# Optimization experiments

Hardware: AMD Instinct MI355X
Metric: run time of the kernel (lower is better)

Reference implementation:

```python
import jax, jax.numpy as jnp
import numpy as np

NUM_TOKENS = 4096
LATENT_DIM = 256
BETA = 0.25
TEMPERATURE = 1.0  # temp_init buffer value
EPS_TEMP = 1e-6


def setup_inputs() -> dict:
    key = jax.random.key(0)
    k1, k2 = jax.random.split(key)
    latent = jax.random.normal(k1, (4, 2048, LATENT_DIM), dtype=jnp.float32)
    cb = jax.random.normal(k2, (NUM_TOKENS, LATENT_DIM), dtype=jnp.float32)
    # module normalizes codebook rows at init
    codebook = cb / jnp.linalg.norm(cb, axis=-1, keepdims=True)
    return {"latent": latent, "codebook": codebook}


def _l2norm(x):
    return x / jnp.clip(jnp.linalg.norm(x, axis=-1, keepdims=True), 1e-12)


def reference(latent, codebook):
    B, S, D = latent.shape
    flat = latent.reshape(-1, D)                       # [N, D]
    # cosine similarity via normalized matmul
    ln = _l2norm(flat)
    cn = _l2norm(codebook)
    cosine_sim = jnp.einsum('nd,kd->nk', ln, cn)       # [N, K]
    distances = 2.0 - 2.0 * cosine_sim
    scaled = distances / jnp.maximum(TEMPERATURE, EPS_TEMP)
    soft_assign = jax.nn.softmax(-scaled, axis=-1)     # [N, K]
    indices = jnp.argmax(soft_assign, axis=-1)         # [N]
    hard_assign = jax.nn.one_hot(indices, NUM_TOKENS, dtype=jnp.float32)
    # straight-through soft->hard assignment
    assign = hard_assign + soft_assign - jax.lax.stop_gradient(soft_assign)

    selected_cosine_sim = jnp.take_along_axis(cosine_sim, indices[:, None], axis=1).mean()

    # codebook pairwise euclidean diagnostics (off-diagonal mean / min)
    sq = jnp.sum(codebook * codebook, axis=-1)         # [K]
    d2 = sq[:, None] + sq[None, :] - 2.0 * (codebook @ codebook.T)
    cdist = jnp.sqrt(jnp.clip(d2, 0.0))                # [K, K]
    K = NUM_TOKENS
    off_sum = jnp.sum(cdist) - jnp.sum(jnp.diagonal(cdist))
    avg_euclidean = off_sum / (K * (K - 1))
    eye = jnp.eye(K, dtype=bool)
    min_euclidean = jnp.min(jnp.where(eye, jnp.inf, cdist))

    quantized = (assign @ codebook).reshape(B, S, D)
    commitment_loss = BETA * jnp.mean((jax.lax.stop_gradient(latent) - quantized) ** 2)
    codebook_loss = jnp.mean((latent - jax.lax.stop_gradient(quantized)) ** 2)
    quantized = latent + jax.lax.stop_gradient(quantized - latent)

    avg_probs = jnp.mean(hard_assign, axis=0)
    perplexity = jnp.exp(-jnp.sum(avg_probs * jnp.log(avg_probs + 1e-10)))

    return (quantized, indices, commitment_loss, codebook_loss, perplexity,
            selected_cosine_sim, avg_euclidean, min_euclidean)
```

## Files before the change

kernel.cpp:

```cpp
#include <hip/hip_runtime.h>
#include <hip/hip_bf16.h>
#include <math.h>

#define NTOK 8192
#define DIM 256
#define KCB 4096
#define NCB (KCB / 128)
#define NKEY 4
#define NKROW (NCB * NKEY)
#define DELTA 0.08f
#define GTIE 2e-6
#define MAXC 16
#define NPAIRB (NCB * (NCB + 1) / 2)
#define NSCOB (NCB * (NTOK / 128))

typedef unsigned long long ull;
typedef unsigned short ushort;
typedef __attribute__((ext_vector_type(8))) short shortx8;
typedef __attribute__((ext_vector_type(4))) float floatx4;
typedef const __attribute__((address_space(1))) void* gas_cp;
typedef __attribute__((address_space(3))) void* las_p;

__device__ __forceinline__ unsigned f2ord(float f) {
    unsigned u = __float_as_uint(f);
    return (u & 0x80000000u) ? ~u : (u | 0x80000000u);
}
__device__ __forceinline__ float ord2f(unsigned u) {
    unsigned b = (u & 0x80000000u) ? (u & 0x7FFFFFFFu) : ~u;
    return __uint_as_float(b);
}
__device__ __forceinline__ ushort f2bf(float f) {
    unsigned u = __float_as_uint(f);
    unsigned r = u + 0x7FFFu + ((u >> 16) & 1u);
    return (ushort)(r >> 16);
}

union TileSmem {
    struct { ushort a[128][64]; ushort b[128][64]; } t;
    unsigned keys[128][33];
    struct { float rs[128]; float rm[128]; } red;
};

__device__ __forceinline__ void stage_tile(const ushort* __restrict__ gbase,
                                           ushort (*lds)[64], int wave, int lane,
                                           int kk) {
    int p = lane & 7;
    int rsub = lane >> 3;
    int kc = p ^ (rsub & 7);
    const ushort* src0 = gbase + (size_t)(wave * 64 + rsub) * DIM + kk + kc * 8;
#pragma unroll
    for (int c = 0; c < 8; ++c) {
        const ushort* src = src0 + (size_t)(c * 8) * DIM;
        __builtin_amdgcn_global_load_lds((gas_cp)src, (las_p)&lds[wave * 64 + c * 8][0],
                                         16, 0, 0);
    }
}
__device__ __forceinline__ shortx8 frag_read(const ushort (*lds)[64], int row,
                                             int lc) {
    return *(const shortx8*)&lds[row][(lc ^ (row & 7)) * 8];
}

__device__ __forceinline__ float np_combine(const float* racc) {
    float h0 = __fadd_rn(__fadd_rn(__fadd_rn(racc[0], racc[1]), __fadd_rn(racc[2], racc[3])),
                         __fadd_rn(__fadd_rn(racc[4], racc[5]), __fadd_rn(racc[6], racc[7])));
    float h1 = __fadd_rn(__fadd_rn(__fadd_rn(racc[8], racc[9]), __fadd_rn(racc[10], racc[11])),
                         __fadd_rn(__fadd_rn(racc[12], racc[13]), __fadd_rn(racc[14], racc[15])));
    float s = __fadd_rn(h0, h1);
    return fmaxf(sqrtf(s), 1e-12f);
}

__global__ __launch_bounds__(256) void prep(const float* __restrict__ lat,
                                            const float* __restrict__ cb,
                                            float* __restrict__ nrml,
                                            float* __restrict__ nrmc,
                                            ushort* __restrict__ latbf,
                                            ushort* __restrict__ cnbf,
                                            ushort* __restrict__ cbbf,
                                            float* __restrict__ sq,
                                            unsigned* __restrict__ counts) {
    int bid = blockIdx.x, t = threadIdx.x;
    if (bid < NTOK) {
        int n = bid;
        if (n < KCB / 256) counts[n * 256 + t] = 0u;
        const float* row = lat + (size_t)n * DIM;
        latbf[(size_t)n * DIM + t] = f2bf(row[t]);
        __shared__ float racc[16];
        if (t < 16) {
            int h = t >> 3, j = t & 7;
            const float* p = row + h * 128;
            float r = __fmul_rn(p[j], p[j]);
#pragma unroll 1
            for (int i = 8; i < 128; i += 8)
                r = __fadd_rn(r, __fmul_rn(p[i + j], p[i + j]));
            racc[t] = r;
        }
        __syncthreads();
        if (t == 0) nrml[n] = np_combine(racc);
    } else {
        int n = bid - NTOK;
        __shared__ float racc2[16];
        __shared__ double dacc[16];
        __shared__ float snrm;
        const float* row = cb + (size_t)n * DIM;
        if (t < 16) {
            int h = t >> 3, j = t & 7;
            const float* p = row + h * 128;
            float r = __fmul_rn(p[j], p[j]);
            double ds = 0.0;
#pragma unroll 1
            for (int i = 8; i < 128; i += 8)
                r = __fadd_rn(r, __fmul_rn(p[i + j], p[i + j]));
#pragma unroll 1
            for (int i = 0; i < 128; i += 8) { double v = (double)p[i + j]; ds += v * v; }
            racc2[t] = r; dacc[t] = ds;
        }
        __syncthreads();
        if (t == 0) {
            float nr = np_combine(racc2);
            snrm = nr; nrmc[n] = nr;
            double ds = 0.0;
            for (int i = 0; i < 16; ++i) ds += dacc[i];
            sq[n] = (float)ds;
        }
        __syncthreads();
        float c = row[t];
        cnbf[(size_t)n * DIM + t] = f2bf(c / snrm);
        cbbf[(size_t)n * DIM + t] = f2bf(c);
    }
}

__global__ __launch_bounds__(128, 2) void gemms(const ushort* __restrict__ latbf,
                                                const ushort* __restrict__ cnbf,
                                                const ushort* __restrict__ cbbf,
                                                const float* __restrict__ sq,
                                                unsigned* __restrict__ keysw,
                                                float* __restrict__ psumw,
                                                unsigned* __restrict__ pminw) {
    __shared__ TileSmem sm;
    int tid = threadIdx.x;
    int wave = tid >> 6, lane = tid & 63;
    int quad = lane >> 4, l15 = lane & 15;
    int wrow = wave * 64;
    bool isScore = blockIdx.x < NSCOB;
    int rowBase, colBase, tri = 0;
    const ushort *gA, *gB;
    if (isScore) {
        int cbk = blockIdx.x & (NCB - 1);
        int rbk = blockIdx.x >> 5;
        rowBase = rbk * 128; colBase = cbk * 128;
        gA = latbf + (size_t)rowBase * DIM;
        gB = cnbf + (size_t)colBase * DIM;
    } else {
        tri = blockIdx.x - NSCOB;
        int a = (int)((sqrtf(8.f * tri + 1.f) - 1.f) * 0.5f);
        while ((a + 1) * (a + 2) / 2 <= tri) ++a;
        while (a * (a + 1) / 2 > tri) --a;
        int b = tri - a * (a + 1) / 2;
        rowBase = b * 128; colBase = a * 128;
        gA = cbbf + (size_t)rowBase * DIM;
        gB = cbbf + (size_t)colBase * DIM;
    }
    floatx4 acc[4][8];
#pragma unroll
    for (int m = 0; m < 4; ++m)
#pragma unroll
        for (int n = 0; n < 8; ++n) acc[m][n] = (floatx4){0.f, 0.f, 0.f, 0.f};
#pragma unroll 1
    for (int kk = 0; kk < DIM; kk += 64) {
        __syncthreads();
        stage_tile(gA, sm.t.a, wave, lane, kk);
        stage_tile(gB, sm.t.b, wave, lane, kk);
        __syncthreads();
#pragma unroll
        for (int s = 0; s < 2; ++s) {
            shortx8 af[4];
#pragma unroll
            for (int mt = 0; mt < 4; ++mt)
                af[mt] = frag_read(sm.t.a, wrow + mt * 16 + l15, s * 4 + quad);
#pragma unroll
            for (int nt = 0; nt < 8; ++nt) {
                shortx8 bfr = frag_read(sm.t.b, nt * 16 + l15, s * 4 + quad);
#pragma unroll
                for (int mt = 0; mt < 4; ++mt)
                    acc[mt][nt] = __builtin_amdgcn_mfma_f32_16x16x32_bf16(
                        af[mt], bfr, acc[mt][nt], 0, 0, 0);
            }
        }
    }
    __syncthreads();
    if (isScore) {
        unsigned colp[8];
#pragma unroll
        for (int nt = 0; nt < 8; ++nt)
            colp[nt] = 4095u - (unsigned)(colBase + nt * 16 + l15);
#pragma unroll
        for (int mt = 0; mt < 4; ++mt)
#pragma unroll
            for (int reg = 0; reg < 4; ++reg) {
                unsigned b1 = 0u, b2 = 0u;
#pragma unroll
                for (int nt = 0; nt < 8; ++nt) {
                    unsigned key = (f2ord(acc[mt][nt][reg]) & 0xFFFFF000u) | colp[nt];
                    unsigned lo = min(key, b1);
                    b1 = max(key, b1);
                    b2 = max(lo, b2);
                }
                int row = wrow + mt * 16 + quad * 4 + reg;
                uint2 kv; kv.x = b1; kv.y = b2;
                *(uint2*)&sm.keys[row][l15 * 2] = kv;
            }
        __syncthreads();
        {
            unsigned a0 = 0, a1 = 0, a2 = 0, a3 = 0;
#pragma unroll
            for (int j = 0; j < 8; ++j) {
                uint4 v4 = *(const uint4*)&sm.keys[tid][j * 4];
                unsigned vs[4] = {v4.x, v4.y, v4.z, v4.w};
#pragma unroll
                for (int q = 0; q < 4; ++q) {
                    unsigned v = vs[q];
                    unsigned n0 = min(v, a0); a0 = max(v, a0);
                    unsigned n1 = min(n0, a1); a1 = max(n0, a1);
                    unsigned n2 = min(n1, a2); a2 = max(n1, a2);
                    a3 = max(n2, a3);
                }
            }
            size_t base = (size_t)(rowBase + tid) * NKROW + (blockIdx.x & (NCB - 1)) * NKEY;
            uint4 o; o.x = a0; o.y = a1; o.z = a2; o.w = a3;
            *(uint4*)&keysw[base] = o;
        }
    } else {
        float lsum = 0.f, lmin = INFINITY;
#pragma unroll
        for (int mt = 0; mt < 4; ++mt)
#pragma unroll
            for (int reg = 0; reg < 4; ++reg) {
                int i = rowBase + wrow + mt * 16 + quad * 4 + reg;
                float sqi = sq[i];
#pragma unroll
                for (int nt = 0; nt < 8; ++nt) {
                    int j = colBase + nt * 16 + l15;
                    float d2 = sqi + sq[j] - 2.0f * acc[mt][nt][reg];
                    float d = sqrtf(fmaxf(d2, 0.0f));
                    bool use = i < j;
                    lsum += use ? d : 0.f;
                    lmin = fminf(lmin, use ? d : INFINITY);
                }
            }
        sm.red.rs[tid] = lsum; sm.red.rm[tid] = lmin; __syncthreads();
        for (int s = 64; s > 0; s >>= 1) {
            if (tid < s) {
                sm.red.rs[tid] += sm.red.rs[tid + s];
                sm.red.rm[tid] = fminf(sm.red.rm[tid], sm.red.rm[tid + s]);
            }
            __syncthreads();
        }
        if (tid == 0) { psumw[tri] = sm.red.rs[0]; pminw[tri] = f2ord(sm.red.rm[0]); }
    }
}

__global__ __launch_bounds__(256) void argmax_resolve(const float* __restrict__ lat,
                                                      const float* __restrict__ cb,
                                                      const float* __restrict__ nrml,
                                                      const float* __restrict__ nrmc,
                                                      const unsigned* __restrict__ keysw,
                                                      float* __restrict__ outidx,
                                                      float* __restrict__ outq,
                                                      unsigned* __restrict__ counts,
                                                      float* __restrict__ selw,
                                                      float* __restrict__ msew) {
    __shared__ int scand[4][MAXC];
    __shared__ double sc64[4][MAXC];
    int wid = threadIdx.x >> 6, lane = threadIdx.x & 63;
    int n = blockIdx.x * 4 + wid;
    const unsigned* kr = keysw + (size_t)n * NKROW;
    uint2 kv = *(const uint2*)(kr + lane * 2);
    unsigned m = max(kv.x, kv.y);
#pragma unroll
    for (int off = 1; off < 64; off <<= 1) {
        unsigned o = __shfl_xor(m, off, 64);
        m = max(m, o);
    }
    float v1 = ord2f(m & 0xFFFFF000u);
    float thresh = v1 - DELTA;
    bool p0 = ord2f(kv.x & 0xFFFFF000u) >= thresh;
    bool p1 = ord2f(kv.y & 0xFFFFF000u) >= thresh;
    ull b0 = __ballot(p0), b1 = __ballot(p1);
    int below0 = __builtin_amdgcn_mbcnt_hi((unsigned)(b0 >> 32),
                 __builtin_amdgcn_mbcnt_lo((unsigned)b0, 0));
    int below1 = __builtin_amdgcn_mbcnt_hi((unsigned)(b1 >> 32),
                 __builtin_amdgcn_mbcnt_lo((unsigned)b1, 0));
    int base1 = __popcll(b0);
    int nc = base1 + __popcll(b1);
    if (p0 && below0 < MAXC)
        scand[wid][below0] = 4095 - (int)(kv.x & 0xFFFu);
    if (p1 && base1 + below1 < MAXC)
        scand[wid][base1 + below1] = 4095 - (int)(kv.y & 0xFFFu);
    nc = nc < MAXC ? nc : MAXC;
    __threadfence_block();
    float nx = nrml[n];
    int d0 = lane * 4;
    float4 xv = *(const float4*)(lat + (size_t)n * DIM + d0);
    int idx; float selcos;
    if (nc <= 1) {
        idx = 4095 - (int)(m & 0xFFFu);
        selcos = v1 / nx;
    } else {
        float la0 = xv.x / nx, la1 = xv.y / nx, la2 = xv.z / nx, la3 = xv.w / nx;
        for (int c = 0; c < nc; ++c) {
            int k = scand[wid][c];
            float nk = nrmc[k];
            float4 cv = *(const float4*)(cb + (size_t)k * DIM + d0);
            double part = (double)(cv.x / nk) * la0 + (double)(cv.y / nk) * la1 +
                          (double)(cv.z / nk) * la2 + (double)(cv.w / nk) * la3;
#pragma unroll
            for (int off = 1; off < 64; off <<= 1) part += __shfl_xor(part, off, 64);
            if (lane == 0) sc64[wid][c] = part;
        }
        __threadfence_block();
        double best64 = -1e300;
        for (int c = 0; c < nc; ++c) best64 = fmax(best64, sc64[wid][c]);
        int nrisk = 0;
        for (int c = 0; c < nc; ++c) if (sc64[wid][c] >= best64 - GTIE) ++nrisk;
        if (nrisk == 1) {
            idx = 0x7FFFFFFF; selcos = 0.f;
            for (int c = 0; c < nc; ++c)
                if (sc64[wid][c] >= best64 - GTIE) { idx = scand[wid][c]; selcos = (float)sc64[wid][c]; }
        } else {
            ull keyf = 0ull, keym = 0ull;
            if (lane < nc && sc64[wid][lane] >= best64 - GTIE) {
                int k = scand[wid][lane];
                const float* cr = cb + (size_t)k * DIM;
                const float* x = lat + (size_t)n * DIM;
                float nk = nrmc[k];
                float af = 0.f, am = 0.f;
                for (int d = 0; d < DIM; ++d) {
                    float la = x[d] / nx;
                    float cv = cr[d] / nk;
                    af = fmaf(la, cv, af);
                    am = __fadd_rn(am, __fmul_rn(la, cv));
                }
                float df = __fsub_rn(2.0f, __fmul_rn(2.0f, af));
                float dm = __fsub_rn(2.0f, __fmul_rn(2.0f, am));
                keyf = ((ull)(0xFFFFFFFFu - f2ord(df)) << 32) | (ull)(0xFFFFFFFFu - (unsigned)k);
                keym = ((ull)(0xFFFFFFFFu - f2ord(dm)) << 32) | (ull)(0xFFFFFFFFu - (unsigned)k);
            }
#pragma unroll
            for (int off = 1; off < 64; off <<= 1) {
                ull of = __shfl_xor(keyf, off, 64);
                ull om = __shfl_xor(keym, off, 64);
                keyf = of > keyf ? of : keyf;
                keym = om > keym ? om : keym;
            }
            int colf = (int)(0xFFFFFFFFu - (unsigned)(keyf & 0xFFFFFFFFull));
            int colm = (int)(0xFFFFFFFFu - (unsigned)(keym & 0xFFFFFFFFull));
            idx = colf < colm ? colf : colm;
            selcos = 0.f;
            for (int c = 0; c < nc; ++c)
                if (scand[wid][c] == idx) selcos = (float)sc64[wid][c];
        }
    }
    float4 qv = *(const float4*)(cb + (size_t)idx * DIM + d0);
    *(float4*)(outq + (size_t)n * DIM + d0) = qv;
    float dx = xv.x - qv.x, dy = xv.y - qv.y, dz = xv.z - qv.z, dw = xv.w - qv.w;
    float msep = fmaf(dx, dx, fmaf(dy, dy, fmaf(dz, dz, dw * dw)));
#pragma unroll
    for (int off = 1; off < 64; off <<= 1) msep += __shfl_xor(msep, off, 64);
    if (lane == 0) {
        outidx[n] = (float)idx;
        atomicAdd(&counts[idx], 1u);
        selw[n] = selcos;
        msew[n] = msep;
    }
}

__global__ void finalize(const unsigned* __restrict__ counts,
                         const float* __restrict__ selw,
                         const float* __restrict__ msew,
                         const float* __restrict__ psumw,
                         const unsigned* __restrict__ pminw,
                         float* __restrict__ outs) {
    int t = threadIdx.x;
    __shared__ float red[256];
    float h = 0.f;
    for (int k = t; k < KCB; k += 256) {
        float p = (float)counts[k] * (1.0f / (float)NTOK);
        h += p * logf(p + 1e-10f);
    }
    red[t] = h; __syncthreads();
    for (int s = 128; s > 0; s >>= 1) { if (t < s) red[t] += red[t + s]; __syncthreads(); }
    float entNeg = red[0];
    __syncthreads();
    float ssel = 0.f;
    for (int k = t; k < NTOK; k += 256) ssel += selw[k];
    red[t] = ssel; __syncthreads();
    for (int s = 128; s > 0; s >>= 1) { if (t < s) red[t] += red[t + s]; __syncthreads(); }
    float selSum = red[0];
    __syncthreads();
    float sm = 0.f;
    for (int k = t; k < NTOK; k += 256) sm += msew[k];
    red[t] = sm; __syncthreads();
    for (int s = 128; s > 0; s >>= 1) { if (t < s) red[t] += red[t + s]; __syncthreads(); }
    float mseSum = red[0];
    __syncthreads();
    float ps = 0.f;
    for (int k = t; k < NPAIRB; k += 256) ps += psumw[k];
    red[t] = ps; __syncthreads();
    for (int s = 128; s > 0; s >>= 1) { if (t < s) red[t] += red[t + s]; __syncthreads(); }
    float pairSum = red[0];
    __syncthreads();
    unsigned pm = 0xFFFFFFFFu;
    for (int k = t; k < NPAIRB; k += 256) pm = min(pm, pminw[k]);
    ((unsigned*)red)[t] = pm; __syncthreads();
    for (int s = 128; s > 0; s >>= 1) {
        if (t < s) ((unsigned*)red)[t] = min(((unsigned*)red)[t], ((unsigned*)red)[t + s]);
        __syncthreads();
    }
    unsigned pairMin = ((unsigned*)red)[0];
    if (t == 0) {
        float mse = mseSum / (float)(NTOK * DIM);
        outs[0] = 0.25f * mse;
        outs[1] = mse;
        outs[2] = expf(-entNeg);
        outs[3] = selSum / (float)NTOK;
        outs[4] = pairSum * 2.0f / ((float)KCB * (float)(KCB - 1));
        outs[5] = ord2f(pairMin);
    }
}

extern "C" void kernel_launch(void* const* d_in, const int* in_sizes, int n_in,
                              void* d_out, int out_size, void* d_ws, size_t ws_size,
                              hipStream_t stream) {
    const float* latent = (const float*)d_in[0];
    const float* codebook = (const float*)d_in[1];
    float* out = (float*)d_out;
    float* outq = out;
    float* outidx = out + (size_t)NTOK * DIM;
    float* outs = outidx + NTOK;

    unsigned* keysw = (unsigned*)d_ws;
    ushort* latbf = (ushort*)(keysw + (size_t)NKROW * NTOK);
    ushort* cnbf = latbf + (size_t)NTOK * DIM;
    ushort* cbbf = cnbf + (size_t)KCB * DIM;
    float* nrml = (float*)(cbbf + (size_t)KCB * DIM);
    float* nrmc = nrml + NTOK;
    float* sq = nrmc + KCB;
    unsigned* counts = (unsigned*)(sq + KCB);
    float* selw = (float*)(counts + KCB);
    float* msew = selw + NTOK;
    float* psumw = msew + NTOK;
    unsigned* pminw = (unsigned*)(psumw + NPAIRB);

    hipLaunchKernelGGL(prep, dim3(NTOK + KCB), dim3(256), 0, stream,
                       latent, codebook, nrml, nrmc, latbf, cnbf, cbbf, sq, counts);
    hipLaunchKernelGGL(gemms, dim3(NSCOB + NPAIRB), dim3(128), 0, stream,
                       latbf, cnbf, cbbf, sq, keysw, psumw, pminw);
    hipLaunchKernelGGL(argmax_resolve, dim3(NTOK / 4), dim3(256), 0, stream,
                       latent, codebook, nrml, nrmc, keysw, outidx, outq, counts, selw, msew);
    hipLaunchKernelGGL(finalize, dim3(1), dim3(256), 0, stream, counts, selw, msew, psumw, pminw, outs);
}
```

Baseline: 177.0 us.

## Split GEMM tile across four waves in a 2x2 layout with a simpler key encoding

The fused score and pairwise-distance GEMM kernel moves from 128 threads (two waves, each computing 64x128) to 256 threads (four waves in a 2x2 grid, each computing 64x64). This halves the accumulator registers per wave and allows more resident waves per CU, which should hide latency better. Tile staging interleaves the A and B loads, and the top-4 key reduction gains an extra LDS merge step across the two column halves. The score key now clamps negative similarities to zero and uses the raw float bits, which is cheaper than the order-preserving transform. The cost is that all negative scores tie and fall back to column order, which is only harmless while each row has enough positive candidates.

```diff
diff --git a/kernel.cpp b/kernel.cpp
--- a/kernel.cpp
+++ b/kernel.cpp
@@ -37,22 +37,25 @@
 
 union TileSmem {
     struct { ushort a[128][64]; ushort b[128][64]; } t;
-    unsigned keys[128][33];
-    struct { float rs[128]; float rm[128]; } red;
+    unsigned keys[128][67];
+    struct { float rs[256]; float rm[256]; } red;
 };
 
-__device__ __forceinline__ void stage_tile(const ushort* __restrict__ gbase,
-                                           ushort (*lds)[64], int wave, int lane,
-                                           int kk) {
+__device__ __forceinline__ void stage_tile4(const ushort* __restrict__ gA,
+                                            const ushort* __restrict__ gB,
+                                            ushort (*la)[64], ushort (*lb)[64],
+                                            int wave, int lane, int kk) {
     int p = lane & 7;
     int rsub = lane >> 3;
-    int kc = p ^ (rsub & 7);
-    const ushort* src0 = gbase + (size_t)(wave * 64 + rsub) * DIM + kk + kc * 8;
-#pragma unroll
-    for (int c = 0; c < 8; ++c) {
-        const ushort* src = src0 + (size_t)(c * 8) * DIM;
-        __builtin_amdgcn_global_load_lds((gas_cp)src, (las_p)&lds[wave * 64 + c * 8][0],
-                                         16, 0, 0);
+    int kc = p ^ rsub;
+    const ushort* sa = gA + (size_t)(wave * 32 + rsub) * DIM + kk + kc * 8;
+    const ushort* sb = gB + (size_t)(wave * 32 + rsub) * DIM + kk + kc * 8;
+#pragma unroll
+    for (int c = 0; c < 4; ++c) {
+        __builtin_amdgcn_global_load_lds((gas_cp)(sa + (size_t)(c * 8) * DIM),
+                                         (las_p)&la[wave * 32 + c * 8][0], 16, 0, 0);
+        __builtin_amdgcn_global_load_lds((gas_cp)(sb + (size_t)(c * 8) * DIM),
+                                         (las_p)&lb[wave * 32 + c * 8][0], 16, 0, 0);
     }
 }
 __device__ __forceinline__ shortx8 frag_read(const ushort (*lds)[64], int row,
@@ -129,7 +132,7 @@
     }
 }
 
-__global__ __launch_bounds__(128, 2) void gemms(const ushort* __restrict__ latbf,
+__global__ __launch_bounds__(256, 3) void gemms(const ushort* __restrict__ latbf,
                                                 const ushort* __restrict__ cnbf,
                                                 const ushort* __restrict__ cbbf,
                                                 const float* __restrict__ sq,
@@ -140,7 +143,7 @@
     int tid = threadIdx.x;
     int wave = tid >> 6, lane = tid & 63;
     int quad = lane >> 4, l15 = lane & 15;
-    int wrow = wave * 64;
+    int wr = wave >> 1, wc = wave & 1;
     bool isScore = blockIdx.x < NSCOB;
     int rowBase, colBase, tri = 0;
     const ushort *gA, *gB;
@@ -160,61 +163,63 @@
         gA = cbbf + (size_t)rowBase * DIM;
         gB = cbbf + (size_t)colBase * DIM;
     }
-    floatx4 acc[4][8];
+    floatx4 acc[4][4];
 #pragma unroll
     for (int m = 0; m < 4; ++m)
 #pragma unroll
-        for (int n = 0; n < 8; ++n) acc[m][n] = (floatx4){0.f, 0.f, 0.f, 0.f};
+        for (int n = 0; n < 4; ++n) acc[m][n] = (floatx4){0.f, 0.f, 0.f, 0.f};
 #pragma unroll 1
     for (int kk = 0; kk < DIM; kk += 64) {
         __syncthreads();
-        stage_tile(gA, sm.t.a, wave, lane, kk);
-        stage_tile(gB, sm.t.b, wave, lane, kk);
+        stage_tile4(gA, gB, sm.t.a, sm.t.b, wave, lane, kk);
         __syncthreads();
 #pragma unroll
         for (int s = 0; s < 2; ++s) {
-            shortx8 af[4];
+            shortx8 af[4], bfv[4];
 #pragma unroll
             for (int mt = 0; mt < 4; ++mt)
-                af[mt] = frag_read(sm.t.a, wrow + mt * 16 + l15, s * 4 + quad);
-#pragma unroll
-            for (int nt = 0; nt < 8; ++nt) {
-                shortx8 bfr = frag_read(sm.t.b, nt * 16 + l15, s * 4 + quad);
-#pragma unroll
-                for (int mt = 0; mt < 4; ++mt)
+                af[mt] = frag_read(sm.t.a, wr * 64 + mt * 16 + l15, s * 4 + quad);
+#pragma unroll
+            for (int nt = 0; nt < 4; ++nt)
+                bfv[nt] = frag_read(sm.t.b, wc * 64 + nt * 16 + l15, s * 4 + quad);
+#pragma unroll
+            for (int mt = 0; mt < 4; ++mt)
+#pragma unroll
+                for (int nt = 0; nt < 4; ++nt)
                     acc[mt][nt] = __builtin_amdgcn_mfma_f32_16x16x32_bf16(
-                        af[mt], bfr, acc[mt][nt], 0, 0, 0);
-            }
+                        af[mt], bfv[nt], acc[mt][nt], 0, 0, 0);
         }
     }
     __syncthreads();
     if (isScore) {
-        unsigned colp[8];
-#pragma unroll
-        for (int nt = 0; nt < 8; ++nt)
-            colp[nt] = 4095u - (unsigned)(colBase + nt * 16 + l15);
+        unsigned colp2[4];
+#pragma unroll
+        for (int nt = 0; nt < 4; ++nt)
+            colp2[nt] = 0x80000000u | (4095u - (unsigned)(colBase + wc * 64 + nt * 16 + l15));
 #pragma unroll
         for (int mt = 0; mt < 4; ++mt)
 #pragma unroll
             for (int reg = 0; reg < 4; ++reg) {
                 unsigned b1 = 0u, b2 = 0u;
 #pragma unroll
-                for (int nt = 0; nt < 8; ++nt) {
-                    unsigned key = (f2ord(acc[mt][nt][reg]) & 0xFFFFF000u) | colp[nt];
+                for (int nt = 0; nt < 4; ++nt) {
+                    unsigned key = (__float_as_uint(fmaxf(acc[mt][nt][reg], 0.f)) & 0x7FFFF000u)
+                                   | colp2[nt];
                     unsigned lo = min(key, b1);
                     b1 = max(key, b1);
                     b2 = max(lo, b2);
                 }
-                int row = wrow + mt * 16 + quad * 4 + reg;
+                int row = wr * 64 + mt * 16 + quad * 4 + reg;
                 uint2 kv; kv.x = b1; kv.y = b2;
-                *(uint2*)&sm.keys[row][l15 * 2] = kv;
+                *(uint2*)&sm.keys[row][(wc * 16 + l15) * 2] = kv;
             }
         __syncthreads();
         {
+            int prow = tid >> 1, ph = tid & 1;
             unsigned a0 = 0, a1 = 0, a2 = 0, a3 = 0;
 #pragma unroll
             for (int j = 0; j < 8; ++j) {
-                uint4 v4 = *(const uint4*)&sm.keys[tid][j * 4];
+                uint4 v4 = *(const uint4*)&sm.keys[prow][ph * 32 + j * 4];
                 unsigned vs[4] = {v4.x, v4.y, v4.z, v4.w};
 #pragma unroll
                 for (int q = 0; q < 4; ++q) {
@@ -225,9 +230,24 @@
                     a3 = max(n2, a3);
                 }
             }
-            size_t base = (size_t)(rowBase + tid) * NKROW + (blockIdx.x & (NCB - 1)) * NKEY;
-            uint4 o; o.x = a0; o.y = a1; o.z = a2; o.w = a3;
-            *(uint4*)&keysw[base] = o;
+            uint4 mine; mine.x = a0; mine.y = a1; mine.z = a2; mine.w = a3;
+            *(uint4*)&sm.keys[prow][ph * 32] = mine;
+            __syncthreads();
+            if (ph == 0) {
+                uint4 o4 = *(const uint4*)&sm.keys[prow][32];
+                unsigned vs[4] = {o4.x, o4.y, o4.z, o4.w};
+#pragma unroll
+                for (int q = 0; q < 4; ++q) {
+                    unsigned v = vs[q];
+                    unsigned n0 = min(v, a0); a0 = max(v, a0);
+                    unsigned n1 = min(n0, a1); a1 = max(n0, a1);
+                    unsigned n2 = min(n1, a2); a2 = max(n1, a2);
+                    a3 = max(n2, a3);
+                }
+                size_t base = (size_t)(rowBase + prow) * NKROW + (blockIdx.x & (NCB - 1)) * NKEY;
+                uint4 o; o.x = a0; o.y = a1; o.z = a2; o.w = a3;
+                *(uint4*)&keysw[base] = o;
+            }
         }
     } else {
         float lsum = 0.f, lmin = INFINITY;
@@ -235,11 +255,11 @@
         for (int mt = 0; mt < 4; ++mt)
 #pragma unroll
             for (int reg = 0; reg < 4; ++reg) {
-                int i = rowBase + wrow + mt * 16 + quad * 4 + reg;
+                int i = rowBase + wr * 64 + mt * 16 + quad * 4 + reg;
                 float sqi = sq[i];
 #pragma unroll
-                for (int nt = 0; nt < 8; ++nt) {
-                    int j = colBase + nt * 16 + l15;
+                for (int nt = 0; nt < 4; ++nt) {
+                    int j = colBase + wc * 64 + nt * 16 + l15;
                     float d2 = sqi + sq[j] - 2.0f * acc[mt][nt][reg];
                     float d = sqrtf(fmaxf(d2, 0.0f));
                     bool use = i < j;
@@ -248,7 +268,7 @@
                 }
             }
         sm.red.rs[tid] = lsum; sm.red.rm[tid] = lmin; __syncthreads();
-        for (int s = 64; s > 0; s >>= 1) {
+        for (int s = 128; s > 0; s >>= 1) {
             if (tid < s) {
                 sm.red.rs[tid] += sm.red.rs[tid + s];
                 sm.red.rm[tid] = fminf(sm.red.rm[tid], sm.red.rm[tid + s]);
@@ -453,7 +473,7 @@
 
     hipLaunchKernelGGL(prep, dim3(NTOK + KCB), dim3(256), 0, stream,
                        latent, codebook, nrml, nrmc, latbf, cnbf, cbbf, sq, counts);
-    hipLaunchKernelGGL(gemms, dim3(NSCOB + NPAIRB), dim3(128), 0, stream,
+    hipLaunchKernelGGL(gemms, dim3(NSCOB + NPAIRB), dim3(256), 0, stream,
                        latbf, cnbf, cbbf, sq, keysw, psumw, pminw);
     hipLaunchKernelGGL(argmax_resolve, dim3(NTOK / 4), dim3(256), 0, stream,
                        latent, codebook, nrml, nrmc, keysw, outidx, outq, counts, selw, msew);
```

Measured after the change: 173.0 us. -2.2%, faster.
